# Optimization experiments

Measured on AMD Instinct MI355X. Metric: run time of the kernel, lower is better.

Reference implementation:

```python
import jax, jax.numpy as jnp
import numpy as np

N, P, Q, H_DIM, HEADS, D = 4096, 128, 128, 256, 8, 64  # D = graph_dim // heads


def setup_inputs() -> dict:
    key = jax.random.key(0)
    ks = jax.random.split(key, 6)
    s = 0.05  # small scale to keep tanh/softmax in a sane range
    return {
        "x_prices": jax.random.normal(ks[0], (N, P), jnp.float32),
        "x_news": jax.random.normal(ks[1], (N, Q), jnp.float32),
        "W_bil": jax.random.normal(ks[2], (H_DIM, P, Q), jnp.float32) * s,
        "b_bil": jax.random.normal(ks[3], (H_DIM,), jnp.float32) * s,
        "Wt": jax.random.normal(ks[4], (HEADS, D, H_DIM), jnp.float32) * s,
        "a_vec": jax.random.normal(ks[5], (HEADS, 2 * D), jnp.float32) * s,
    }


def reference(x_prices, x_news, W_bil, b_bil, Wt, a_vec):
    # nn.Bilinear: out[n,h] = sum_pq x_prices[n,p] W[h,p,q] x_news[n,q] + b[h]
    x = jnp.einsum('np,hpq,nq->nh', x_prices, W_bil, x_news) + b_bil  # (N, hidden)

    # Per-head linear transform: fc_transform (no bias). Wt: (heads, d, hidden)
    xt = jnp.einsum('nh,kdh->knd', x, Wt)  # (heads, N, d)

    # Attention score a . [x_i, x_j] split into src/dst halves -> broadcast add
    d = Wt.shape[1]
    a_src, a_dst = a_vec[:, :d], a_vec[:, d:]
    s_src = jnp.einsum('knd,kd->kn', xt, a_src)  # (heads, N)
    s_dst = jnp.einsum('knd,kd->kn', xt, a_dst)  # (heads, N)
    scores = s_src[:, :, None] + s_dst[:, None, :]  # (heads, N, N)
    scores = jnp.where(scores >= 0, scores, 0.2 * scores)  # LeakyReLU(0.2)

    attn = jax.nn.softmax(scores, axis=-1)  # softmax over neighbors j
    out = jnp.einsum('knm,kmd->knd', attn, xt)  # (heads, N, d)

    # Concatenate head outputs on feature dim, then tanh
    out = jnp.transpose(out, (1, 0, 2)).reshape(xt.shape[1], -1)  # (N, heads*d)
    return jnp.tanh(out)
```

## Files before the change

### kernel.cpp

```cpp
#include <hip/hip_runtime.h>
#include <hip/hip_bf16.h>

typedef unsigned short ushort;
typedef unsigned int uint;
typedef unsigned long long u64;
typedef _Float16 f16;

#define NN 4096
#define PP 128
#define QQ 128
#define HD 256
#define KH 8
#define DD 64
#define KK 16384

typedef _Float16 f16x2 __attribute__((ext_vector_type(2)));
typedef _Float16 f16x4 __attribute__((ext_vector_type(4)));
typedef _Float16 f16x8 __attribute__((ext_vector_type(8)));
typedef __fp16 fp16x2 __attribute__((ext_vector_type(2)));
typedef float f32x4 __attribute__((ext_vector_type(4)));

__device__ inline void async_lds16(const void* g, void* l) {
  __builtin_amdgcn_global_load_lds(
      (const __attribute__((address_space(1))) unsigned int*)g,
      (__attribute__((address_space(3))) unsigned int*)l, 16, 0, 0);
}

__global__ __launch_bounds__(256) void k0_split2(
    const float* __restrict__ W, const float* __restrict__ Wt,
    f16* __restrict__ hiW, f16* __restrict__ loW,
    f16* __restrict__ hiT, f16* __restrict__ loT, float* __restrict__ xz) {
  const int tid = blockIdx.x * 256 + threadIdx.x;
  const int i = tid * 4;
  if (tid < (NN * HD) / 4)
    *(float4*)&xz[i] = make_float4(0.f, 0.f, 0.f, 0.f);
  const float* src;
  f16 *hi, *lo;
  int off;
  if (i < HD * PP * QQ) { src = W; hi = hiW; lo = loW; off = i; }
  else { src = Wt; hi = hiT; lo = loT; off = i - HD * PP * QQ; }
  const float4 w = *(const float4*)&src[off];
  const float wf[4] = {w.x, w.y, w.z, w.w};
  f16x4 hv, lv;
#pragma unroll
  for (int j = 0; j < 4; ++j) {
    const f16 h = (f16)wf[j];
    hv[j] = h;
    lv[j] = (f16)(wf[j] - (float)h);
  }
  *(f16x4*)&hi[off] = hv;
  *(f16x4*)&lo[off] = lv;
}

__global__ __launch_bounds__(256, 4) void k1_bilinear(
    const float* __restrict__ xp, const float* __restrict__ xn,
    const f16* __restrict__ Whi, const f16* __restrict__ Wlo,
    float* __restrict__ xout) {
  __shared__ f16 whi[2][128 * 32];
  __shared__ f16 wlo[2][128 * 32];
  __shared__ f16 zhi[128 * 32];

  const int t = threadIdx.x;
  const int bid = blockIdx.x;
  const int xcd = bid & 7, slot = bid >> 3;
  const int jpan = slot >> 5, n_idx = slot & 31;
  const int pan = xcd + 8 * jpan;
  const int n0 = n_idx * 128;
  const int kb = (pan & 15) * (KK / 16);
  const int h0 = (pan >> 4) * 128;
  const int pb = kb >> 7;

  const int l = t & 63, w = t >> 6;
  const int wr = (w >> 1) * 64, wc = (w & 1) * 64;

  int aoff[4], boff[4];
#pragma unroll
  for (int i = 0; i < 4; ++i) {
    const int row = wr + i * 16 + (l & 15);
    aoff[i] = row * 32 + (((l >> 4) ^ ((row ^ (row >> 2)) & 3)) * 8);
  }
#pragma unroll
  for (int j = 0; j < 4; ++j) {
    const int hr = wc + j * 16 + (l & 15);
    boff[j] = hr * 32 + (((l >> 4) ^ ((hr ^ (hr >> 2)) & 3)) * 8);
  }

  const int shb = t >> 2, seg = t & 3;
  int gsw[2];
#pragma unroll
  for (int g = 0; g < 2; ++g) {
    const int r = shb + 64 * g;
    gsw[g] = seg ^ ((r ^ (r >> 2)) & 3);
  }

  auto stage_w = [&](int buf, int kc_) {
#pragma unroll
    for (int g = 0; g < 2; ++g) {
      const int r = shb + 64 * g;
      async_lds16(Whi + (size_t)(h0 + r) * KK + kc_ + gsw[g] * 8,
                  &whi[buf][r * 32 + seg * 8]);
      async_lds16(Wlo + (size_t)(h0 + r) * KK + kc_ + gsw[g] * 8,
                  &wlo[buf][r * 32 + seg * 8]);
    }
  };

  const int zn = t >> 1, zko = (t & 1) * 16;
  const int zm = (zn ^ (zn >> 2)) & 3;
  const int zs0 = (t & 1) * 2;
  const int zo0 = zn * 32 + ((zs0 ^ zm) * 8);
  const int zo1 = zn * 32 + (((zs0 + 1) ^ zm) * 8);

  f32x4 acc[4][4];
#pragma unroll
  for (int i = 0; i < 4; ++i)
#pragma unroll
    for (int j = 0; j < 4; ++j) acc[i][j] = (f32x4)0.f;

  float xpp[8];
  {
    const float* xpr = xp + (size_t)(n0 + zn) * PP + pb;
    const f32x4 a = *(const f32x4*)xpr;
    const f32x4 b = *(const f32x4*)(xpr + 4);
    xpp[0] = a[0]; xpp[1] = a[1]; xpp[2] = a[2]; xpp[3] = a[3];
    xpp[4] = b[0]; xpp[5] = b[1]; xpp[6] = b[2]; xpp[7] = b[3];
  }
  const float* xrow = xn + (size_t)(n0 + zn) * QQ + zko;
  float4 xv0 = ((const float4*)xrow)[0];
  float4 xv1 = ((const float4*)xrow)[1];
  float4 xv2 = ((const float4*)xrow)[2];
  float4 xv3 = ((const float4*)xrow)[3];
  stage_w(0, kb);
  __syncthreads();

#pragma unroll
  for (int pl = 0; pl < 8; ++pl) {
#pragma unroll 1
    for (int q = 0; q < 4; ++q) {
      const int c = pl * 4 + q;
      const int cur = c & 1;
      const bool more = (pl < 7) || (q < 3);

      asm volatile("s_waitcnt lgkmcnt(0)" ::: "memory");
      __builtin_amdgcn_sched_barrier(0);
      __builtin_amdgcn_s_barrier();
      __builtin_amdgcn_sched_barrier(0);

      if (more) stage_w(cur ^ 1, kb + (c + 1) * 32);

      {
        const float xpv = xpp[pl];
        float zz[16] = {xv0.x, xv0.y, xv0.z, xv0.w, xv1.x, xv1.y, xv1.z, xv1.w,
                        xv2.x, xv2.y, xv2.z, xv2.w, xv3.x, xv3.y, xv3.z, xv3.w};
        union { uint u[8]; uint4 qd[2]; } ph;
#pragma unroll
        for (int j = 0; j < 8; ++j) {
          union { fp16x2 h; uint u; } cv;
          cv.h = __builtin_amdgcn_cvt_pkrtz(xpv * zz[2 * j], xpv * zz[2 * j + 1]);
          ph.u[j] = cv.u;
        }
        *(uint4*)&zhi[zo0] = ph.qd[0];
        *(uint4*)&zhi[zo1] = ph.qd[1];
      }

      asm volatile("s_waitcnt lgkmcnt(0)" ::: "memory");
      __builtin_amdgcn_sched_barrier(0);
      __builtin_amdgcn_s_barrier();
      __builtin_amdgcn_sched_barrier(0);

      if (more) {
        const int qn = ((c + 1) & 3) * 32;
        xv0 = ((const float4*)(xrow + qn))[0];
        xv1 = ((const float4*)(xrow + qn))[1];
        xv2 = ((const float4*)(xrow + qn))[2];
        xv3 = ((const float4*)(xrow + qn))[3];
      }

      f16x8 Ah[4];
#pragma unroll
      for (int i = 0; i < 4; ++i) Ah[i] = *(const f16x8*)&zhi[aoff[i]];
#pragma unroll
      for (int j = 0; j < 4; ++j) {
        const f16x8 Bh = *(const f16x8*)&whi[cur][boff[j]];
        const f16x8 Bl = *(const f16x8*)&wlo[cur][boff[j]];
#pragma unroll
        for (int i = 0; i < 4; ++i)
          acc[i][j] = __builtin_amdgcn_mfma_f32_16x16x32_f16(Ah[i], Bh, acc[i][j], 0, 0, 0);
#pragma unroll
        for (int i = 0; i < 4; ++i)
          acc[i][j] = __builtin_amdgcn_mfma_f32_16x16x32_f16(Ah[i], Bl, acc[i][j], 0, 0, 0);
      }
    }
  }

#pragma unroll
  for (int i = 0; i < 4; ++i)
#pragma unroll
    for (int j = 0; j < 4; ++j) {
      const int row = n0 + wr + i * 16 + (l >> 4) * 4;
      const int col = h0 + wc + j * 16 + (l & 15);
#pragma unroll
      for (int r = 0; r < 4; ++r)
        atomicAdd(&xout[(size_t)(row + r) * HD + col], acc[i][j][r]);
    }
}

__global__ __launch_bounds__(256) void k23_xt(
    const float* __restrict__ x, const float* __restrict__ bb,
    const f16* __restrict__ Wthi, const f16* __restrict__ Wtlo,
    const float* __restrict__ av, float* __restrict__ xt,
    float* __restrict__ ssrc, float* __restrict__ sdst) {
  __shared__ f16 ah[64 * 32];
  __shared__ f16 bh[128 * 32];
  __shared__ f16 bl[128 * 32];
  __shared__ float red1[2][64][17];
  __shared__ float red2[2][64][17];
  const int t = threadIdx.x;
  const int n0 = blockIdx.x * 64;
  const int c0 = blockIdx.y * 128;
  const int l = t & 63, w = t >> 6;
  const int wn = (w & 1) * 32, wcc = (w >> 1) * 64;

  int aoff[2], boff[4];
#pragma unroll
  for (int i = 0; i < 2; ++i) {
    const int row = wn + i * 16 + (l & 15);
    aoff[i] = row * 32 + (((l >> 4) ^ ((row ^ (row >> 2)) & 3)) * 8);
  }
#pragma unroll
  for (int j = 0; j < 4; ++j) {
    const int hr = wcc + j * 16 + (l & 15);
    boff[j] = hr * 32 + (((l >> 4) ^ ((hr ^ (hr >> 2)) & 3)) * 8);
  }

  f32x4 acc[2][4];
#pragma unroll
  for (int i = 0; i < 2; ++i)
#pragma unroll
    for (int j = 0; j < 4; ++j) acc[i][j] = (f32x4)0.f;

  for (int kc = 0; kc < HD; kc += 32) {
    __syncthreads();
    {
      const int row = t >> 2, sg = t & 3;
      const float* xr = &x[(size_t)(n0 + row) * HD + kc + sg * 8];
      const float4 xa = ((const float4*)xr)[0];
      const float4 xb = ((const float4*)xr)[1];
      const float4 ba = *(const float4*)&bb[kc + sg * 8];
      const float4 bv = *(const float4*)&bb[kc + sg * 8 + 4];
      f16x8 o;
      o[0] = (f16)(xa.x + ba.x); o[1] = (f16)(xa.y + ba.y);
      o[2] = (f16)(xa.z + ba.z); o[3] = (f16)(xa.w + ba.w);
      o[4] = (f16)(xb.x + bv.x); o[5] = (f16)(xb.y + bv.y);
      o[6] = (f16)(xb.z + bv.z); o[7] = (f16)(xb.w + bv.w);
      const int sgs = sg ^ ((row ^ (row >> 2)) & 3);
      *(f16x8*)&ah[row * 32 + sgs * 8] = o;
    }
#pragma unroll
    for (int g = 0; g < 2; ++g) {
      const int slot = g * 256 + t;
      const int col = slot >> 2, ps = slot & 3;
      const int ls = ps ^ ((col ^ (col >> 2)) & 3);
      *(uint4*)&bh[col * 32 + ps * 8] =
          *(const uint4*)&Wthi[(size_t)(c0 + col) * HD + kc + ls * 8];
      *(uint4*)&bl[col * 32 + ps * 8] =
          *(const uint4*)&Wtlo[(size_t)(c0 + col) * HD + kc + ls * 8];
    }
    __syncthreads();
    f16x8 Af[2];
#pragma unroll
    for (int i = 0; i < 2; ++i) Af[i] = *(const f16x8*)&ah[aoff[i]];
#pragma unroll
    for (int j = 0; j < 4; ++j) {
      const f16x8 Bh = *(const f16x8*)&bh[boff[j]];
      const f16x8 Bl = *(const f16x8*)&bl[boff[j]];
#pragma unroll
      for (int i = 0; i < 2; ++i)
        acc[i][j] = __builtin_amdgcn_mfma_f32_16x16x32_f16(Af[i], Bh, acc[i][j], 0, 0, 0);
#pragma unroll
      for (int i = 0; i < 2; ++i)
        acc[i][j] = __builtin_amdgcn_mfma_f32_16x16x32_f16(Af[i], Bl, acc[i][j], 0, 0, 0);
    }
  }

  const int hh = w >> 1;
  const int khead = (c0 >> 6) + hh;
  float a1v[4], a2v[4];
#pragma unroll
  for (int j = 0; j < 4; ++j) {
    const int d = j * 16 + (l & 15);
    a1v[j] = av[khead * (2 * DD) + d];
    a2v[j] = av[khead * (2 * DD) + DD + d];
  }

#pragma unroll
  for (int i = 0; i < 2; ++i)
#pragma unroll
    for (int r = 0; r < 4; ++r) {
      const int rowl = wn + i * 16 + (l >> 4) * 4 + r;
      float p1 = 0.f, p2 = 0.f;
#pragma unroll
      for (int j = 0; j < 4; ++j) {
        p1 += acc[i][j][r] * a1v[j];
        p2 += acc[i][j][r] * a2v[j];
      }
      red1[hh][rowl][l & 15] = p1;
      red2[hh][rowl][l & 15] = p2;
    }

#pragma unroll
  for (int i = 0; i < 2; ++i)
#pragma unroll
    for (int j = 0; j < 4; ++j) {
      const int row = n0 + wn + i * 16 + (l >> 4) * 4;
      const int colg = c0 + wcc + j * 16 + (l & 15);
      const int k = colg >> 6, d = colg & 63;
#pragma unroll
      for (int r = 0; r < 4; ++r)
        xt[((size_t)(k * NN + row + r)) * DD + d] = acc[i][j][r];
    }

  __syncthreads();
  {
    const int hh2 = t >> 7;
    const int which = (t >> 6) & 1;
    const int row = t & 63;
    const float* rp = which ? &red2[hh2][row][0] : &red1[hh2][row][0];
    float s = 0.f;
#pragma unroll
    for (int g = 0; g < 16; ++g) s += rp[g];
    const int kk = (c0 >> 6) + hh2;
    if (which) sdst[kk * NN + n0 + row] = s;
    else ssrc[kk * NN + n0 + row] = s;
  }
}

__global__ __launch_bounds__(256) void k4_rank(
    const float* __restrict__ sdst, float* __restrict__ vsorted,
    int* __restrict__ perm) {
  __shared__ u64 kv[4096];
  __shared__ ushort pcnt[256];
  const int k = blockIdx.y, t = threadIdx.x;
  for (int i = t; i < 4096; i += 256) {
    const uint u = __float_as_uint(sdst[k * NN + i]);
    const uint key = (u & 0x80000000u) ? ~u : (u | 0x80000000u);
    kv[i] = ((u64)key << 32) | (uint)i;
  }
  __syncthreads();
  const int idx = t & 127;
  const int half = t >> 7;
  const u64 my = kv[blockIdx.x * 128 + idx];
  const int j0 = half * 2048;
  int cnt = 0;
#pragma unroll 16
  for (int j = 0; j < 2048; ++j) cnt += (kv[j0 + j] < my) ? 1 : 0;
  pcnt[t] = (ushort)cnt;
  __syncthreads();
  if (t < 128) {
    const int tot = (int)pcnt[t] + (int)pcnt[t + 128];
    const u64 my2 = kv[blockIdx.x * 128 + t];
    const uint key = (uint)(my2 >> 32);
    const uint u = (key & 0x80000000u) ? (key ^ 0x80000000u) : ~key;
    vsorted[k * NN + tot] = __uint_as_float(u);
    perm[k * NN + tot] = (int)(my2 & 0xFFFFFFFFu);
  }
}

__global__ __launch_bounds__(64) void k4b_chunksum(
    const float* __restrict__ vs, const int* __restrict__ perm,
    const float* __restrict__ xt, float* __restrict__ Chi, float* __restrict__ Clo) {
  __shared__ float rows[64][64];
  __shared__ float eh[64], el[64];
  const int c = blockIdx.x, k = blockIdx.y, t = threadIdx.x;
  const int base = k * NN + c * 64;
  {
    const float v = vs[base + t];
    eh[t] = __expf(v);
    el[t] = __expf(0.2f * v);
  }
#pragma unroll
  for (int r = 0; r < 16; ++r) {
    const int i = r * 4 + (t >> 4);
    const int p = perm[base + i];
    *(float4*)&rows[i][(t & 15) * 4] =
        *(const float4*)&xt[((size_t)(k * NN + p)) * DD + (t & 15) * 4];
  }
  __syncthreads();
  float shi = 0.f, slo = 0.f, whs = 0.f, wls = 0.f;
#pragma unroll 8
  for (int i = 0; i < 64; ++i) {
    const float val = rows[i][t];
    shi += eh[i] * val; slo += el[i] * val;
    whs += eh[i]; wls += el[i];
  }
  const int cb = (k * 64 + c) * 65;
  Chi[cb + t] = shi;
  Clo[cb + t] = slo;
  if (t == 0) { Chi[cb + 64] = whs; Clo[cb + 64] = wls; }
}

__global__ __launch_bounds__(64) void k4d_expand(
    const float* __restrict__ vs, const int* __restrict__ perm,
    const float* __restrict__ xt, const float* __restrict__ Chi,
    const float* __restrict__ Clo, float* __restrict__ Phi,
    float* __restrict__ Plo) {
  __shared__ float scs[64 * 65];
  __shared__ float rows[64][64];
  __shared__ float ev[64];
  const int c = blockIdx.x, k = blockIdx.y, t = threadIdx.x;
  const int pass = blockIdx.z;
  const int base = k * NN + c * 64;
  const float* Cs = pass ? Chi : Clo;
  for (int idx = t; idx < 4160; idx += 64) scs[idx] = Cs[k * 4160 + idx];
  {
    const float v = vs[base + t];
    ev[t] = pass ? __expf(v) : __expf(0.2f * v);
  }
#pragma unroll
  for (int r = 0; r < 16; ++r) {
    const int i = r * 4 + (t >> 4);
    const int p = perm[base + i];
    *(float4*)&rows[i][(t & 15) * 4] =
        *(const float4*)&xt[((size_t)(k * NN + p)) * DD + (t & 15) * 4];
  }
  __syncthreads();

  if (pass == 0) {
    float run = 0.f, wrun = 0.f;
    for (int cc = 0; cc < c; ++cc) {
      run += scs[cc * 65 + t];
      wrun += scs[cc * 65 + 64];
    }
    for (int i = 0; i < 64; ++i) {
      const size_t rb = ((size_t)(k * 4097) + c * 64 + i) * 65;
      Plo[rb + t] = run;
      if (t == 0) Plo[rb + 64] = wrun;
      run += ev[i] * rows[i][t];
      wrun += ev[i];
    }
    if (c == 63) {
      const size_t rb = ((size_t)(k * 4097) + 4096) * 65;
      Plo[rb + t] = run;
      if (t == 0) Plo[rb + 64] = wrun;
    }
  } else {
    float runS = 0.f, wrunS = 0.f;
    for (int cc = c + 1; cc < 64; ++cc) {
      runS += scs[cc * 65 + t];
      wrunS += scs[cc * 65 + 64];
    }
    for (int i = 63; i >= 0; --i) {
      runS += ev[i] * rows[i][t];
      wrunS += ev[i];
      const size_t rb = ((size_t)(k * 4097) + c * 64 + i) * 65;
      Phi[rb + t] = runS;
      if (t == 0) Phi[rb + 64] = wrunS;
    }
    if (c == 63) {
      const size_t rb = ((size_t)(k * 4097) + 4096) * 65;
      Phi[rb + t] = 0.f;
      if (t == 0) Phi[rb + 64] = 0.f;
    }
  }
}

__global__ __launch_bounds__(256) void k6_final(
    const float* __restrict__ ssrc, const float* __restrict__ vsorted,
    const float* __restrict__ Phi, const float* __restrict__ Plo,
    float* __restrict__ out) {
  __shared__ float vsh[4096];
  __shared__ int posSh[16];
  const int t = threadIdx.x;
  const int q0 = blockIdx.x * 16;
  const int k = q0 >> 12;
  for (int idx = t; idx < 1024; idx += 256)
    *(float4*)&vsh[idx * 4] = *(const float4*)&vsorted[k * NN + idx * 4];
  __syncthreads();
  if (t < 16) {
    const float thr = -ssrc[q0 + t];
    int lo = 0, hi = 4096;
    while (lo < hi) {
      const int mid = (lo + hi) >> 1;
      if (vsh[mid] < thr) lo = mid + 1; else hi = mid;
    }
    posSh[t] = lo;
  }
  __syncthreads();
  const int d = t & 63;
#pragma unroll
  for (int qq = 0; qq < 4; ++qq) {
    const int ql = qq * 4 + (t >> 6);
    const int qi = q0 + ql;
    const int n = qi & 4095;
    const float u = ssrc[qi];
    const size_t rb = ((size_t)(k * 4097) + posSh[ql]) * 65;
    const float eu = __expf(u), el = __expf(0.2f * u);
    const float num = eu * Phi[rb + d] + el * Plo[rb + d];
    const float den = eu * Phi[rb + 64] + el * Plo[rb + 64];
    out[(size_t)n * (KH * DD) + k * DD + d] = tanhf(num / den);
  }
}

extern "C" void kernel_launch(void* const* d_in, const int* in_sizes, int n_in,
                              void* d_out, int out_size, void* d_ws, size_t ws_size,
                              hipStream_t stream) {
  const float* xp = (const float*)d_in[0];
  const float* xn = (const float*)d_in[1];
  const float* W = (const float*)d_in[2];
  const float* bb = (const float*)d_in[3];
  const float* Wt = (const float*)d_in[4];
  const float* av = (const float*)d_in[5];
  float* out = (float*)d_out;

  char* ws = (char*)d_ws;
  f16* Whi    = (f16*)(ws);
  f16* Wlo    = (f16*)(ws + 8388608);
  float* Phi  = (float*)(ws);
  float* Plo  = (float*)(ws + 8522240);
  float* x    = (float*)(ws + 17044480);
  float* xt   = (float*)(ws + 21238784);
  f16* Wthi   = (f16*)(ws + 31724544);
  f16* Wtlo   = (f16*)(ws + 31986688);
  float* ssrc = (float*)(ws + 32248832);
  float* sdst = (float*)(ws + 32379904);
  float* vsort= (float*)(ws + 32510976);
  int*   perm = (int*)  (ws + 32642048);
  float* Chi  = (float*)(ws + 32773120);
  float* Clo  = (float*)(ws + 32906240);

  k0_split2<<<(HD * PP * QQ + KH * DD * HD) / 1024, 256, 0, stream>>>(
      W, Wt, Whi, Wlo, Wthi, Wtlo, x);
  k1_bilinear<<<1024, 256, 0, stream>>>(xp, xn, Whi, Wlo, x);
  k23_xt<<<dim3(NN / 64, 4), 256, 0, stream>>>(x, bb, Wthi, Wtlo, av, xt, ssrc, sdst);
  k4_rank<<<dim3(32, KH), 256, 0, stream>>>(sdst, vsort, perm);
  k4b_chunksum<<<dim3(64, KH), 64, 0, stream>>>(vsort, perm, xt, Chi, Clo);
  k4d_expand<<<dim3(64, KH, 2), 64, 0, stream>>>(vsort, perm, xt, Chi, Clo, Phi, Plo);
  k6_final<<<(KH * NN) / 16, 256, 0, stream>>>(ssrc, vsort, Phi, Plo, out);
}
```

Before: 243.8 us.

## Halve bilinear N-tile and double-buffer Z tile to drop one barrier per step

```diff
diff --git a/kernel.cpp b/kernel.cpp
--- a/kernel.cpp
+++ b/kernel.cpp
@@ -58,30 +58,30 @@
     float* __restrict__ xout) {
   __shared__ f16 whi[2][128 * 32];
   __shared__ f16 wlo[2][128 * 32];
-  __shared__ f16 zhi[128 * 32];
+  __shared__ f16 zhi[2][64 * 32];
 
   const int t = threadIdx.x;
   const int bid = blockIdx.x;
   const int xcd = bid & 7, slot = bid >> 3;
-  const int jpan = slot >> 5, n_idx = slot & 31;
+  const int jpan = slot >> 6, n_idx = slot & 63;
   const int pan = xcd + 8 * jpan;
-  const int n0 = n_idx * 128;
+  const int n0 = n_idx * 64;
   const int kb = (pan & 15) * (KK / 16);
   const int h0 = (pan >> 4) * 128;
   const int pb = kb >> 7;
 
   const int l = t & 63, w = t >> 6;
-  const int wr = (w >> 1) * 64, wc = (w & 1) * 64;
-
-  int aoff[4], boff[4];
-#pragma unroll
-  for (int i = 0; i < 4; ++i) {
-    const int row = wr + i * 16 + (l & 15);
+  const int wn = (w & 1) * 32, wh = (w >> 1) * 64;
+
+  int aoff[2], boff[4];
+#pragma unroll
+  for (int i = 0; i < 2; ++i) {
+    const int row = wn + i * 16 + (l & 15);
     aoff[i] = row * 32 + (((l >> 4) ^ ((row ^ (row >> 2)) & 3)) * 8);
   }
 #pragma unroll
   for (int j = 0; j < 4; ++j) {
-    const int hr = wc + j * 16 + (l & 15);
+    const int hr = wh + j * 16 + (l & 15);
     boff[j] = hr * 32 + (((l >> 4) ^ ((hr ^ (hr >> 2)) & 3)) * 8);
   }
 
@@ -104,17 +104,10 @@
     }
   };
 
-  const int zn = t >> 1, zko = (t & 1) * 16;
+  const int zn = t >> 2, zs = t & 3;
   const int zm = (zn ^ (zn >> 2)) & 3;
-  const int zs0 = (t & 1) * 2;
-  const int zo0 = zn * 32 + ((zs0 ^ zm) * 8);
-  const int zo1 = zn * 32 + (((zs0 + 1) ^ zm) * 8);
-
-  f32x4 acc[4][4];
-#pragma unroll
-  for (int i = 0; i < 4; ++i)
-#pragma unroll
-    for (int j = 0; j < 4; ++j) acc[i][j] = (f32x4)0.f;
+  const int zoff = zn * 32 + ((zs ^ zm) * 8);
+  const float* xrow = xn + (size_t)(n0 + zn) * QQ + zs * 8;
 
   float xpp[8];
   {
@@ -124,80 +117,82 @@
     xpp[0] = a[0]; xpp[1] = a[1]; xpp[2] = a[2]; xpp[3] = a[3];
     xpp[4] = b[0]; xpp[5] = b[1]; xpp[6] = b[2]; xpp[7] = b[3];
   }
-  const float* xrow = xn + (size_t)(n0 + zn) * QQ + zko;
-  float4 xv0 = ((const float4*)xrow)[0];
-  float4 xv1 = ((const float4*)xrow)[1];
-  float4 xv2 = ((const float4*)xrow)[2];
-  float4 xv3 = ((const float4*)xrow)[3];
+
+  f32x4 acc[2][4];
+#pragma unroll
+  for (int i = 0; i < 2; ++i)
+#pragma unroll
+    for (int j = 0; j < 4; ++j) acc[i][j] = (f32x4)0.f;
+
+  f32x4 xa, xb;
+
+  auto form_z = [&](int buf, float xpv) {
+    union { uint u[4]; uint4 q; } ph;
+    union { fp16x2 h; uint uu; } cv;
+    cv.h = __builtin_amdgcn_cvt_pkrtz(xpv * xa[0], xpv * xa[1]); ph.u[0] = cv.uu;
+    cv.h = __builtin_amdgcn_cvt_pkrtz(xpv * xa[2], xpv * xa[3]); ph.u[1] = cv.uu;
+    cv.h = __builtin_amdgcn_cvt_pkrtz(xpv * xb[0], xpv * xb[1]); ph.u[2] = cv.uu;
+    cv.h = __builtin_amdgcn_cvt_pkrtz(xpv * xb[2], xpv * xb[3]); ph.u[3] = cv.uu;
+    *(uint4*)&zhi[buf][zoff] = ph.q;
+  };
+
+  xa = *(const f32x4*)(xrow);
+  xb = *(const f32x4*)(xrow + 4);
+  form_z(0, xpp[0]);
   stage_w(0, kb);
-  __syncthreads();
-
-#pragma unroll
-  for (int pl = 0; pl < 8; ++pl) {
-#pragma unroll 1
-    for (int q = 0; q < 4; ++q) {
-      const int c = pl * 4 + q;
-      const int cur = c & 1;
-      const bool more = (pl < 7) || (q < 3);
-
-      asm volatile("s_waitcnt lgkmcnt(0)" ::: "memory");
+  __builtin_amdgcn_sched_barrier(0);
+  xa = *(const f32x4*)(xrow + 32);
+  xb = *(const f32x4*)(xrow + 36);
+  asm volatile("s_waitcnt vmcnt(2) lgkmcnt(0)" ::: "memory");
+  __builtin_amdgcn_sched_barrier(0);
+  __builtin_amdgcn_s_barrier();
+  __builtin_amdgcn_sched_barrier(0);
+
+#pragma unroll
+  for (int c = 0; c < 32; ++c) {
+    const int cur = c & 1;
+    if (c < 31) stage_w(cur ^ 1, kb + (c + 1) * 32);
+    __builtin_amdgcn_sched_barrier(0);
+
+    if (c < 31) form_z(cur ^ 1, xpp[(c + 1) >> 2]);
+
+    f16x8 Ah[2];
+    Ah[0] = *(const f16x8*)&zhi[cur][aoff[0]];
+    Ah[1] = *(const f16x8*)&zhi[cur][aoff[1]];
+#pragma unroll
+    for (int j = 0; j < 4; ++j) {
+      const f16x8 Bh = *(const f16x8*)&whi[cur][boff[j]];
+      const f16x8 Bl = *(const f16x8*)&wlo[cur][boff[j]];
+      acc[0][j] = __builtin_amdgcn_mfma_f32_16x16x32_f16(Ah[0], Bh, acc[0][j], 0, 0, 0);
+      acc[1][j] = __builtin_amdgcn_mfma_f32_16x16x32_f16(Ah[1], Bh, acc[1][j], 0, 0, 0);
+      acc[0][j] = __builtin_amdgcn_mfma_f32_16x16x32_f16(Ah[0], Bl, acc[0][j], 0, 0, 0);
+      acc[1][j] = __builtin_amdgcn_mfma_f32_16x16x32_f16(Ah[1], Bl, acc[1][j], 0, 0, 0);
+    }
+    __builtin_amdgcn_sched_barrier(0);
+
+    if (c < 30) {
+      const int qn = ((c + 2) & 3) * 32;
+      xa = *(const f32x4*)(xrow + qn);
+      xb = *(const f32x4*)(xrow + qn + 4);
+    }
+
+    if (c < 31) {
+      if (c < 30)
+        asm volatile("s_waitcnt vmcnt(2) lgkmcnt(0)" ::: "memory");
+      else
+        asm volatile("s_waitcnt vmcnt(0) lgkmcnt(0)" ::: "memory");
       __builtin_amdgcn_sched_barrier(0);
       __builtin_amdgcn_s_barrier();
       __builtin_amdgcn_sched_barrier(0);
-
-      if (more) stage_w(cur ^ 1, kb + (c + 1) * 32);
-
-      {
-        const float xpv = xpp[pl];
-        float zz[16] = {xv0.x, xv0.y, xv0.z, xv0.w, xv1.x, xv1.y, xv1.z, xv1.w,
-                        xv2.x, xv2.y, xv2.z, xv2.w, xv3.x, xv3.y, xv3.z, xv3.w};
-        union { uint u[8]; uint4 qd[2]; } ph;
-#pragma unroll
-        for (int j = 0; j < 8; ++j) {
-          union { fp16x2 h; uint u; } cv;
-          cv.h = __builtin_amdgcn_cvt_pkrtz(xpv * zz[2 * j], xpv * zz[2 * j + 1]);
-          ph.u[j] = cv.u;
-        }
-        *(uint4*)&zhi[zo0] = ph.qd[0];
-        *(uint4*)&zhi[zo1] = ph.qd[1];
-      }
-
-      asm volatile("s_waitcnt lgkmcnt(0)" ::: "memory");
-      __builtin_amdgcn_sched_barrier(0);
-      __builtin_amdgcn_s_barrier();
-      __builtin_amdgcn_sched_barrier(0);
-
-      if (more) {
-        const int qn = ((c + 1) & 3) * 32;
-        xv0 = ((const float4*)(xrow + qn))[0];
-        xv1 = ((const float4*)(xrow + qn))[1];
-        xv2 = ((const float4*)(xrow + qn))[2];
-        xv3 = ((const float4*)(xrow + qn))[3];
-      }
-
-      f16x8 Ah[4];
-#pragma unroll
-      for (int i = 0; i < 4; ++i) Ah[i] = *(const f16x8*)&zhi[aoff[i]];
-#pragma unroll
-      for (int j = 0; j < 4; ++j) {
-        const f16x8 Bh = *(const f16x8*)&whi[cur][boff[j]];
-        const f16x8 Bl = *(const f16x8*)&wlo[cur][boff[j]];
-#pragma unroll
-        for (int i = 0; i < 4; ++i)
-          acc[i][j] = __builtin_amdgcn_mfma_f32_16x16x32_f16(Ah[i], Bh, acc[i][j], 0, 0, 0);
-#pragma unroll
-        for (int i = 0; i < 4; ++i)
-          acc[i][j] = __builtin_amdgcn_mfma_f32_16x16x32_f16(Ah[i], Bl, acc[i][j], 0, 0, 0);
-      }
-    }
-  }
-
-#pragma unroll
-  for (int i = 0; i < 4; ++i)
+    }
+  }
+
+#pragma unroll
+  for (int i = 0; i < 2; ++i)
 #pragma unroll
     for (int j = 0; j < 4; ++j) {
-      const int row = n0 + wr + i * 16 + (l >> 4) * 4;
-      const int col = h0 + wc + j * 16 + (l & 15);
+      const int row = n0 + wn + i * 16 + (l >> 4) * 4;
+      const int col = h0 + wh + j * 16 + (l & 15);
 #pragma unroll
       for (int r = 0; r < 4; ++r)
         atomicAdd(&xout[(size_t)(row + r) * HD + col], acc[i][j][r]);
@@ -529,7 +524,7 @@
 
   k0_split2<<<(HD * PP * QQ + KH * DD * HD) / 1024, 256, 0, stream>>>(
       W, Wt, Whi, Wlo, Wthi, Wtlo, x);
-  k1_bilinear<<<1024, 256, 0, stream>>>(xp, xn, Whi, Wlo, x);
+  k1_bilinear<<<2048, 256, 0, stream>>>(xp, xn, Whi, Wlo, x);
   k23_xt<<<dim3(NN / 64, 4), 256, 0, stream>>>(x, bb, Wthi, Wtlo, av, xt, ssrc, sdst);
   k4_rank<<<dim3(32, KH), 256, 0, stream>>>(sdst, vsort, perm);
   k4b_chunksum<<<dim3(64, KH), 64, 0, stream>>>(vsort, perm, xt, Chi, Clo);
```

New measurement: 247.3 us. Within noise of the previous version (+1.4%).
